# Performance work log

Hardware: AMD Instinct MI355X
Metric: run time of the kernel (lower is better)

## Reference

```python
import jax, jax.numpy as jnp
import numpy as np

NUM_HEADS = 16
WINDOW = 128

def setup_inputs() -> dict:
    key = jax.random.key(0)
    ks = jax.random.split(key, 9)
    E, B, S = 1024, 2, 2048
    sc = 1.0 / np.sqrt(E)
    return {
        'x':  jax.random.normal(ks[0], (B, S, E), jnp.float32),
        'Wq': jax.random.normal(ks[1], (E, E), jnp.float32) * sc,
        'bq': jax.random.normal(ks[2], (E,), jnp.float32) * 0.02,
        'Wk': jax.random.normal(ks[3], (E, E), jnp.float32) * sc,
        'bk': jax.random.normal(ks[4], (E,), jnp.float32) * 0.02,
        'Wv': jax.random.normal(ks[5], (E, E), jnp.float32) * sc,
        'bv': jax.random.normal(ks[6], (E,), jnp.float32) * 0.02,
        'Wo': jax.random.normal(ks[7], (E, E), jnp.float32) * sc,
        'bo': jax.random.normal(ks[8], (E,), jnp.float32) * 0.02,
    }

def reference(x, Wq, bq, Wk, bk, Wv, bv, Wo, bo):
    B, S, E = x.shape
    H = NUM_HEADS
    D = E // H
    # projections -> [B, H, S, D]
    q = (x @ Wq + bq).reshape(B, S, H, D).transpose(0, 2, 1, 3)
    k = (x @ Wk + bk).reshape(B, S, H, D).transpose(0, 2, 1, 3)
    v = (x @ Wv + bv).reshape(B, S, H, D).transpose(0, 2, 1, 3)
    # dense scores [B, H, S, S]
    energy = jnp.einsum('bhqd,bhkd->bhqk', q, k)
    idx = jnp.arange(S)
    blocked = jnp.abs(idx[:, None] - idx[None, :]) > WINDOW  # True = outside band
    neg = jnp.finfo(jnp.float32).min
    energy = jnp.where(blocked[None, None], neg, energy)
    # note: original scales by sqrt(emb_size), not sqrt(head_dim)
    att = jax.nn.softmax(energy / jnp.sqrt(jnp.float32(E)), axis=-1)
    out = jnp.einsum('bhqk,bhkd->bhqd', att, v)
    out = out.transpose(0, 2, 1, 3).reshape(B, S, E)
    return out @ Wo + bo
```

## Files before the change

### kernel.cpp

```cpp
#include <hip/hip_runtime.h>

typedef unsigned short u16;
typedef unsigned int u32;
typedef __attribute__((ext_vector_type(8))) short bf16x8;
typedef __attribute__((ext_vector_type(4))) float f32x4;
typedef __attribute__((ext_vector_type(4))) unsigned int u32x4;
typedef __attribute__((ext_vector_type(4))) unsigned short u16x4;

#define DEV static __device__ __forceinline__

DEV u16 f2bf(float f) {
  unsigned u = __builtin_bit_cast(unsigned, f);
  u += 0x7FFFu + ((u >> 16) & 1u);
  return (u16)(u >> 16);
}

DEV u32 cvt_pk_bf16(float lo, float hi) {
  u32 d;
  asm("v_cvt_pk_bf16_f32 %0, %1, %2" : "=v"(d) : "v"(lo), "v"(hi));
  return d;
}

DEV void load_lds16(const void* g, void* l) {
  __builtin_amdgcn_global_load_lds(
      (const __attribute__((address_space(1))) unsigned int*)g,
      (__attribute__((address_space(3))) unsigned int*)l, 16, 0, 0);
}


__global__ void k_prep(const float* __restrict__ x,
                       const float* __restrict__ bq, const float* __restrict__ bk,
                       const float* __restrict__ bv,
                       const float* __restrict__ Wq, const float* __restrict__ Wk,
                       const float* __restrict__ Wv, const float* __restrict__ Wo,
                       u16* __restrict__ xb, u16* __restrict__ wtqkv,
                       u16* __restrict__ wto, float* __restrict__ bias) {
  const int tid = threadIdx.x;
  const int bid = blockIdx.x;
  if (bid < 4096) {
    __shared__ float t[32][33];
    const int wi = bid >> 10, inner = bid & 1023;
    const float* W = (wi == 0) ? Wq : (wi == 1) ? Wk : (wi == 2) ? Wv : Wo;
    u16* Wt = (wi == 3) ? wto : wtqkv + (size_t)wi * 1024 * 1024;
    const int tx = tid & 31, ty = tid >> 5;
    const int c0 = (inner & 31) * 32, r0 = (inner >> 5) * 32;
#pragma unroll
    for (int i = 0; i < 4; ++i)
      t[ty + i * 8][tx] = W[(size_t)(r0 + ty + i * 8) * 1024 + c0 + tx];
    __syncthreads();
#pragma unroll
    for (int i = 0; i < 4; ++i)
      Wt[(size_t)(c0 + ty + i * 8) * 1024 + r0 + tx] = f2bf(t[tx][ty + i * 8]);
  } else if (bid < 8192) {
    int i = ((bid - 4096) * 256 + tid) * 4;
    f32x4 v = *(const f32x4*)(x + i);
    u16x4 o;
#pragma unroll
    for (int j = 0; j < 4; ++j) o[j] = f2bf(v[j]);
    *(u16x4*)(xb + i) = o;
  } else {
    int i = (bid - 8192) * 256 + tid;
    float v = (i < 1024) ? bq[i] : (i < 2048) ? bk[i - 1024] : bv[i - 2048];
    bias[i] = v;
  }
}


template <int BN, typename CT>
__launch_bounds__(256, 2) __global__
void k_gemm_bt(const u16* __restrict__ A, const u16* __restrict__ Bt,
               const float* __restrict__ bias, CT* __restrict__ C, int ldc,
               u16* __restrict__ vtp) {
  constexpr int BM = 128, BK = 64;
  constexpr int NJ = BN / 32;
  constexpr int EPW = BN / 2 + 4;
  __shared__ __align__(16) char smem[(BM + BN) * BK * 2];
  u16* lA = (u16*)smem;
  u16* lB = (u16*)(smem + BM * BK * 2);
  float (*ep)[16][EPW] = (float (*)[16][EPW])smem;

  const int tid = threadIdx.x;
  const int w = tid >> 6, lane = tid & 63, g = lane >> 4, n16 = lane & 15;
  const int wm = w >> 1, wn = w & 1;

  const int nbx = gridDim.x;
  const int flat = blockIdx.y * nbx + blockIdx.x;
  const int cpx = (nbx * gridDim.y) >> 3;
  const int swz = (flat & 7) * cpx + (flat >> 3);
  const int m0 = (swz / nbx) * BM, n0 = (swz % nbx) * BN;

#define STAGE(k0)                                                            \
  do {                                                                       \
    _Pragma("unroll")                                                        \
    for (int r = 0; r < BM / 32; ++r) {                                      \
      int s = r * 256 + tid;                                                 \
      int row = s >> 3, cc = (s & 7) ^ (row & 7);                            \
      load_lds16(A + (size_t)(m0 + row) * 1024 + (k0) + cc * 8, lA + s * 8); \
    }                                                                        \
    _Pragma("unroll")                                                        \
    for (int r = 0; r < BN / 32; ++r) {                                      \
      int s = r * 256 + tid;                                                 \
      int row = s >> 3, cc = (s & 7) ^ (row & 7);                            \
      load_lds16(Bt + (size_t)(n0 + row) * 1024 + (k0) + cc * 8, lB + s * 8);\
    }                                                                        \
  } while (0)

  f32x4 acc[4][NJ] = {};
  STAGE(0);
  for (int t = 0; t < 16; ++t) {
    __syncthreads();
    bf16x8 af[2][4], bfr[2][NJ];
#pragma unroll
    for (int kh = 0; kh < 2; ++kh) {
      const int csel = ((kh * 4 + g) ^ (n16 & 7)) * 8;
#pragma unroll
      for (int i = 0; i < 4; ++i)
        af[kh][i] = *(const bf16x8*)&lA[(wm * 64 + i * 16 + n16) * 64 + csel];
#pragma unroll
      for (int j = 0; j < NJ; ++j)
        bfr[kh][j] = *(const bf16x8*)&lB[(wn * (BN / 2) + j * 16 + n16) * 64 + csel];
    }
    __syncthreads();
    if (t < 15) STAGE((t + 1) * 64);
    __builtin_amdgcn_s_setprio(1);
#pragma unroll
    for (int kh = 0; kh < 2; ++kh)
#pragma unroll
      for (int i = 0; i < 4; ++i)
#pragma unroll
        for (int j = 0; j < NJ; ++j)
          acc[i][j] =
              __builtin_amdgcn_mfma_f32_16x16x32_bf16(af[kh][i], bfr[kh][j], acc[i][j], 0, 0, 0);
    __builtin_amdgcn_s_setprio(0);
  }
#undef STAGE
  __syncthreads();

  const int m_base = m0 + wm * 64, n_base = n0 + wn * (BN / 2);
  bool vmode = false;
  if constexpr (sizeof(CT) == 2 && BN == 128)
    vmode = (vtp != nullptr) && (n_base >= 2048);

#pragma unroll
  for (int i = 0; i < 4; ++i) {
#pragma unroll
    for (int j = 0; j < NJ; ++j) {
      float bv = bias[n_base + j * 16 + n16];
#pragma unroll
      for (int jj = 0; jj < 4; ++jj)
        ep[w][g * 4 + jj][j * 16 + n16] = acc[i][j][jj] + bv;
    }
    asm volatile("s_waitcnt lgkmcnt(0)" ::: "memory");
    if (vmode) {
      const int head = (n_base - 2048) >> 6;
      const int m_row0 = m_base + i * 16;
      const int bb = m_row0 >> 11, s0 = m_row0 & 2047;
      union { u16 a[16]; u32x4 v[2]; } pk;
#pragma unroll
      for (int r = 0; r < 16; ++r) pk.a[r] = f2bf(ep[w][r][lane]);
      size_t vrow = ((size_t)(bb * 16 + head) * 64 + lane) * 2048 + s0;
      *(u32x4*)(vtp + vrow) = pk.v[0];
      *(u32x4*)(vtp + vrow + 8) = pk.v[1];
    } else {
      constexpr int CPR = BN / 8;
      constexpr int P = 16 * CPR / 64;
#pragma unroll
      for (int p = 0; p < P; ++p) {
        int fl = p * 64 + lane;
        int row = fl / CPR, cc = (fl % CPR) * 4;
        f32x4 v = *(const f32x4*)&ep[w][row][cc];
        size_t off = (size_t)(m_base + i * 16 + row) * ldc + n_base + cc;
        if constexpr (sizeof(CT) == 2) {
          u16x4 o;
#pragma unroll
          for (int q = 0; q < 4; ++q) o[q] = f2bf(v[q]);
          *(u16x4*)(C + off) = o;
        } else {
          *(f32x4*)(C + off) = v;
        }
      }
    }
    asm volatile("s_waitcnt lgkmcnt(0)" ::: "memory");
  }
}


__launch_bounds__(256, 3) __global__
void k_attn(const u16* __restrict__ qkv, const u16* __restrict__ vt,
            u16* __restrict__ attn) {
  __shared__ __align__(16) u16 KV[20480];
  __shared__ __align__(16) u16 Ostg[4][16][64];
  const int tid = threadIdx.x;
  const int w = tid >> 6, lane = tid & 63, g = lane >> 4, n16 = lane & 15;
  const int bid = (blockIdx.x & 7) * 128 + (blockIdx.x >> 3);
  const int qt = bid & 31, h = (bid >> 5) & 15, b = bid >> 9;
  const int q0b = qt * 64;
  const int kvb = q0b - 128;
  const int q0 = q0b + w * 16;
  const int kv0 = q0 - 128;
  const int q = q0 + n16;
  const int bh = b * 16 + h;

  {
    const u16* kpart = qkv + (size_t)b * 2048 * 3072 + 1024 + h * 64;
#pragma unroll
    for (int i = 0; i < 10; ++i) {
      int c = i * 256 + tid;
      int r = c >> 3, cc = c & 7;
      int srcr = min(max(kvb + r, 0), 2047);
      load_lds16(kpart + (size_t)srcr * 3072 + (cc ^ (r & 7)) * 8, &KV[c * 8]);
    }
  }

  const size_t rowQ = (size_t)(b * 2048 + q) * 3072 + h * 64;
  bf16x8 qf0 = *(const bf16x8*)(qkv + rowQ + g * 8);
  bf16x8 qf1 = *(const bf16x8*)(qkv + rowQ + 32 + g * 8);
  __syncthreads();

  const int kbase = 8 * (n16 >> 2) + (n16 & 3);
  const int wrel = 16 * w;
  f32x4 sv[18];
#pragma unroll
  for (int t = 0; t < 18; ++t) {
    int kr = wrel + 32 * (t >> 1) + 4 * (t & 1) + kbase;
    int krl = min(kr, 319);
    int p = krl & 7;
    const u16* kp = &KV[krl * 64];
    bf16x8 kf0 = *(const bf16x8*)(kp + (g ^ p) * 8);
    bf16x8 kf1 = *(const bf16x8*)(kp + ((g + 4) ^ p) * 8);
    f32x4 s = {0.f, 0.f, 0.f, 0.f};
    s = __builtin_amdgcn_mfma_f32_16x16x32_bf16(kf0, qf0, s, 0, 0, 0);
    s = __builtin_amdgcn_mfma_f32_16x16x32_bf16(kf1, qf1, s, 0, 0, 0);
    sv[t] = s;
  }
  __syncthreads();

  {
    const u16* vpart = vt + (size_t)bh * 64 * 2048;
#pragma unroll
    for (int i = 0; i < 10; ++i) {
      int c = i * 256 + tid;
      int d = c / 40, cc = c - d * 40;
      int j = cc ^ (d & 7);
      int srck = min(max(kvb + j * 8, 0), 2040);
      load_lds16(vpart + (size_t)d * 2048 + srck, &KV[c * 8]);
    }
  }

  const float NEG = -__builtin_inff();
#pragma unroll
  for (int t = 0; t < 18; ++t) {
    int kb = kv0 + 32 * (t >> 1) + 4 * (t & 1) + 8 * g;
#pragma unroll
    for (int jj = 0; jj < 4; ++jj) {
      int k = kb + jj;
      bool ok = ((unsigned)k < 2048u) && ((unsigned)(q - k + 128) <= 256u);
      sv[t][jj] = ok ? sv[t][jj] : NEG;
    }
  }

  float mx = NEG;
#pragma unroll
  for (int t = 0; t < 18; ++t)
    mx = fmaxf(mx, fmaxf(fmaxf(sv[t][0], sv[t][1]), fmaxf(sv[t][2], sv[t][3])));
  mx = fmaxf(mx, __shfl_xor(mx, 16));
  mx = fmaxf(mx, __shfl_xor(mx, 32));

  const float c = 0.04508422017f;
  const float nmc = -mx * c;
  float sum = 0.f;
#pragma unroll
  for (int t = 0; t < 18; ++t)
#pragma unroll
    for (int jj = 0; jj < 4; ++jj) {
      float p = exp2f(fmaf(sv[t][jj], c, nmc));
      sv[t][jj] = p;
      sum += p;
    }
  sum += __shfl_xor(sum, 16);
  sum += __shfl_xor(sum, 32);
  const float inv = 1.f / sum;

  __syncthreads();

  f32x4 oacc[4] = {};
#pragma unroll
  for (int s = 0; s < 9; ++s) {
    union { u32 u[4]; bf16x8 v; } paf;
    paf.u[0] = cvt_pk_bf16(sv[2 * s][0], sv[2 * s][1]);
    paf.u[1] = cvt_pk_bf16(sv[2 * s][2], sv[2 * s][3]);
    paf.u[2] = cvt_pk_bf16(sv[2 * s + 1][0], sv[2 * s + 1][1]);
    paf.u[3] = cvt_pk_bf16(sv[2 * s + 1][2], sv[2 * s + 1][3]);
    int jc = min(2 * w + 4 * s + g, 39);
#pragma unroll
    for (int dt = 0; dt < 4; ++dt) {
      int d = dt * 16 + n16;
      bf16x8 vf = *(const bf16x8*)&KV[d * 320 + (jc ^ (d & 7)) * 8];
      oacc[dt] = __builtin_amdgcn_mfma_f32_16x16x32_bf16(paf.v, vf, oacc[dt], 0, 0, 0);
    }
  }

  float rs[4];
#pragma unroll
  for (int jj = 0; jj < 4; ++jj) rs[jj] = __shfl(inv, 4 * g + jj);

#pragma unroll
  for (int dt = 0; dt < 4; ++dt)
#pragma unroll
    for (int jj = 0; jj < 4; ++jj)
      Ostg[w][g * 4 + jj][dt * 16 + n16] = f2bf(oacc[dt][jj] * rs[jj]);
  asm volatile("s_waitcnt lgkmcnt(0)" ::: "memory");
#pragma unroll
  for (int p = 0; p < 2; ++p) {
    int fl = p * 512 + lane * 8;
    int row = fl >> 6, col = fl & 63;
    u32x4 v = *(const u32x4*)&Ostg[w][row][col];
    *(u32x4*)(attn + (size_t)(b * 2048 + q0 + row) * 1024 + h * 64 + col) = v;
  }
}


extern "C" void kernel_launch(void* const* d_in, const int* in_sizes, int n_in,
                              void* d_out, int out_size, void* d_ws, size_t ws_size,
                              hipStream_t stream) {
  const float* x  = (const float*)d_in[0];
  const float* Wq = (const float*)d_in[1];
  const float* bq = (const float*)d_in[2];
  const float* Wk = (const float*)d_in[3];
  const float* bk = (const float*)d_in[4];
  const float* Wv = (const float*)d_in[5];
  const float* bv = (const float*)d_in[6];
  const float* Wo = (const float*)d_in[7];
  const float* bo = (const float*)d_in[8];

  char* ws = (char*)d_ws;
  const size_t MB = 1ull << 20;
  u16*   xb    = (u16*)(ws + 0);
  u16*   wtqkv = (u16*)(ws + 8 * MB);
  u16*   wto   = (u16*)(ws + 14 * MB);
  float* bias  = (float*)(ws + 16 * MB);
  u16*   qkvb  = (u16*)(ws + 17 * MB);
  u16*   vtb   = (u16*)(ws + 41 * MB);
  u16*   attnb = (u16*)(ws + 0);

  k_prep<<<8204, 256, 0, stream>>>(x, bq, bk, bv, Wq, Wk, Wv, Wo,
                                   xb, wtqkv, wto, bias);
  k_gemm_bt<128, u16><<<dim3(24, 32), 256, 0, stream>>>(xb, wtqkv, bias, qkvb, 3072, vtb);
  k_attn<<<1024, 256, 0, stream>>>(qkvb, vtb, attnb);
  k_gemm_bt<64, float><<<dim3(16, 32), 256, 0, stream>>>(attnb, wto, bo, (float*)d_out,
                                                         1024, nullptr);
}
```

Baseline: 76.35 us.

## Double-buffer GEMM LDS staging and retune K-tile swizzle in attention

New measurement: 74.04 us. 1.03x faster.

```diff
diff --git a/kernel.cpp b/kernel.cpp
--- a/kernel.cpp
+++ b/kernel.cpp
@@ -74,9 +74,9 @@
   constexpr int BM = 128, BK = 64;
   constexpr int NJ = BN / 32;
   constexpr int EPW = BN / 2 + 4;
-  __shared__ __align__(16) char smem[(BM + BN) * BK * 2];
-  u16* lA = (u16*)smem;
-  u16* lB = (u16*)(smem + BM * BK * 2);
+  constexpr int HALF = (BM + BN) * BK * 2;
+  constexpr int LPS = BM / 32 + BN / 32;
+  __shared__ __align__(16) char smem[2 * HALF];
   float (*ep)[16][EPW] = (float (*)[16][EPW])smem;
 
   const int tid = threadIdx.x;
@@ -89,39 +89,52 @@
   const int swz = (flat & 7) * cpx + (flat >> 3);
   const int m0 = (swz / nbx) * BM, n0 = (swz % nbx) * BN;
 
-#define STAGE(k0)                                                            \
-  do {                                                                       \
-    _Pragma("unroll")                                                        \
-    for (int r = 0; r < BM / 32; ++r) {                                      \
-      int s = r * 256 + tid;                                                 \
-      int row = s >> 3, cc = (s & 7) ^ (row & 7);                            \
-      load_lds16(A + (size_t)(m0 + row) * 1024 + (k0) + cc * 8, lA + s * 8); \
-    }                                                                        \
-    _Pragma("unroll")                                                        \
-    for (int r = 0; r < BN / 32; ++r) {                                      \
-      int s = r * 256 + tid;                                                 \
-      int row = s >> 3, cc = (s & 7) ^ (row & 7);                            \
-      load_lds16(Bt + (size_t)(n0 + row) * 1024 + (k0) + cc * 8, lB + s * 8);\
-    }                                                                        \
+#define STAGE(k0, bsel)                                                        \
+  do {                                                                         \
+    u16* lAb = (u16*)(smem + (bsel) * HALF);                                   \
+    u16* lBb = lAb + BM * BK;                                                  \
+    _Pragma("unroll")                                                          \
+    for (int r = 0; r < BM / 32; ++r) {                                        \
+      int s = r * 256 + tid;                                                   \
+      int row = s >> 3, cc = (s & 7) ^ (row & 7);                              \
+      load_lds16(A + (size_t)(m0 + row) * 1024 + (k0) + cc * 8, lAb + s * 8);  \
+    }                                                                          \
+    _Pragma("unroll")                                                          \
+    for (int r = 0; r < BN / 32; ++r) {                                        \
+      int s = r * 256 + tid;                                                   \
+      int row = s >> 3, cc = (s & 7) ^ (row & 7);                              \
+      load_lds16(Bt + (size_t)(n0 + row) * 1024 + (k0) + cc * 8, lBb + s * 8); \
+    }                                                                          \
   } while (0)
 
   f32x4 acc[4][NJ] = {};
-  STAGE(0);
+  STAGE(0, 0);
+  STAGE(64, 1);
+#pragma unroll 2
   for (int t = 0; t < 16; ++t) {
-    __syncthreads();
+    const int buf = t & 1;
+    if (t < 15) {
+      asm volatile("s_waitcnt vmcnt(%0)" ::"n"(LPS) : "memory");
+    } else {
+      asm volatile("s_waitcnt vmcnt(0)" ::: "memory");
+    }
+    __builtin_amdgcn_s_barrier();
+    const u16* lAb = (const u16*)(smem + buf * HALF);
+    const u16* lBb = lAb + BM * BK;
     bf16x8 af[2][4], bfr[2][NJ];
 #pragma unroll
     for (int kh = 0; kh < 2; ++kh) {
       const int csel = ((kh * 4 + g) ^ (n16 & 7)) * 8;
 #pragma unroll
       for (int i = 0; i < 4; ++i)
-        af[kh][i] = *(const bf16x8*)&lA[(wm * 64 + i * 16 + n16) * 64 + csel];
+        af[kh][i] = *(const bf16x8*)&lAb[(wm * 64 + i * 16 + n16) * 64 + csel];
 #pragma unroll
       for (int j = 0; j < NJ; ++j)
-        bfr[kh][j] = *(const bf16x8*)&lB[(wn * (BN / 2) + j * 16 + n16) * 64 + csel];
-    }
-    __syncthreads();
-    if (t < 15) STAGE((t + 1) * 64);
+        bfr[kh][j] = *(const bf16x8*)&lBb[(wn * (BN / 2) + j * 16 + n16) * 64 + csel];
+    }
+    asm volatile("s_waitcnt lgkmcnt(0)" ::: "memory");
+    __builtin_amdgcn_s_barrier();
+    if (t < 14) STAGE((t + 2) * 64, buf);
     __builtin_amdgcn_s_setprio(1);
 #pragma unroll
     for (int kh = 0; kh < 2; ++kh)
@@ -206,9 +219,10 @@
 #pragma unroll
     for (int i = 0; i < 10; ++i) {
       int c = i * 256 + tid;
-      int r = c >> 3, cc = c & 7;
+      int r = c >> 3, sl = c & 7;
+      int m = (r & 3) | (((r >> 3) & 1) << 2);
       int srcr = min(max(kvb + r, 0), 2047);
-      load_lds16(kpart + (size_t)srcr * 3072 + (cc ^ (r & 7)) * 8, &KV[c * 8]);
+      load_lds16(kpart + (size_t)srcr * 3072 + (sl ^ m) * 8, &KV[c * 8]);
     }
   }
 
@@ -224,7 +238,7 @@
   for (int t = 0; t < 18; ++t) {
     int kr = wrel + 32 * (t >> 1) + 4 * (t & 1) + kbase;
     int krl = min(kr, 319);
-    int p = krl & 7;
+    int p = (krl & 3) | (((krl >> 3) & 1) << 2);
     const u16* kp = &KV[krl * 64];
     bf16x8 kf0 = *(const bf16x8*)(kp + (g ^ p) * 8);
     bf16x8 kf1 = *(const bf16x8*)(kp + ((g + 4) ^ p) * 8);
```
